# Kernel optimization log

Measured on AMD Instinct MI355X. Metric: run time of the kernel, lower is better.

Reference implementation:

```python
import jax, jax.numpy as jnp
import numpy as np

H, D = 4, 32          # heads, per-head dim (= hidden_channels)
HD = H * D            # concat width fed between layers
L = 2                 # num HGT layers
OUT = 128             # final output dim
SCALE = 1.0 / np.sqrt(D)


def _seg_softmax(score, seg, n):
    # segment softmax over incoming edges per destination node, per head
    mx = jax.ops.segment_max(score, seg, num_segments=n)
    ex = jnp.exp(score - mx[seg])
    den = jax.ops.segment_sum(ex, seg, num_segments=n)
    return ex / den[seg]


def _hgt_side(q_dst, k_src, v_src, src, dst, a_rel, m_rel, p_rel, n_dst):
    # k/v: [N_src,H,D]; a_rel,m_rel: [H,D,D]; p_rel: [H]
    k_t = jnp.einsum('ehd,hdf->ehf', k_src[src], a_rel)          # [E,H,D]
    score = (q_dst[dst] * k_t).sum(-1) * p_rel * SCALE           # [E,H]
    alpha = _seg_softmax(score, dst, n_dst)                      # [E,H]
    v_t = jnp.einsum('ehd,hdf->ehf', v_src[src], m_rel)          # [E,H,D]
    return jax.ops.segment_sum(alpha[..., None] * v_t, dst, num_segments=n_dst)


def _forward(x_m, x_g, W_in_m, b_in_m, W_in_g, b_in_g,
             Wk_m, bk_m, Wq_m, bq_m, Wv_m, bv_m,
             Wk_g, bk_g, Wq_g, bq_g, Wv_g, bv_g,
             a_mg, m_mg, p_mg, a_gm, m_gm, p_gm,
             Wa_m, ba_m, Wa_g, ba_g, skip_m, skip_g,
             W_out_m, b_out_m, W_out_g, b_out_g,
             edge_mg_src, edge_mg_dst, edge_gm_src, edge_gm_dst):
    Nm, Ng = x_m.shape[0], x_g.shape[0]
    # per-node-type input projection
    h_m = x_m @ W_in_m + b_in_m                                  # [Nm,HD]
    h_g = x_g @ W_in_g + b_in_g                                  # [Ng,HD]
    for l in range(L):
        k_m = (h_m @ Wk_m[l] + bk_m[l]).reshape(Nm, H, D)
        q_m = (h_m @ Wq_m[l] + bq_m[l]).reshape(Nm, H, D)
        v_m = (h_m @ Wv_m[l] + bv_m[l]).reshape(Nm, H, D)
        k_g = (h_g @ Wk_g[l] + bk_g[l]).reshape(Ng, H, D)
        q_g = (h_g @ Wq_g[l] + bq_g[l]).reshape(Ng, H, D)
        v_g = (h_g @ Wv_g[l] + bv_g[l]).reshape(Ng, H, D)
        agg_g = _hgt_side(q_g, k_m, v_m, edge_mg_src, edge_mg_dst,
                          a_mg[l], m_mg[l], p_mg[l], Ng)         # [Ng,H,D]
        agg_m = _hgt_side(q_m, k_g, v_g, edge_gm_src, edge_gm_dst,
                          a_gm[l], m_gm[l], p_gm[l], Nm)         # [Nm,H,D]
        o_m = jax.nn.gelu(agg_m.reshape(Nm, HD), approximate=False) @ Wa_m[l] + ba_m[l]
        o_g = jax.nn.gelu(agg_g.reshape(Ng, HD), approximate=False) @ Wa_g[l] + ba_g[l]
        bm = jax.nn.sigmoid(skip_m[l])
        bg = jax.nn.sigmoid(skip_g[l])
        h_m = jax.nn.elu(bm * o_m + (1.0 - bm) * h_m)            # HGTConv skip, then model-level ELU
        h_g = jax.nn.elu(bg * o_g + (1.0 - bg) * h_g)
    out_m = h_m @ W_out_m + b_out_m                              # [Nm,OUT]
    out_g = h_g @ W_out_g + b_out_g                              # [Ng,OUT]
    return jnp.concatenate([out_m, out_g], axis=0)               # [Nm+Ng,OUT]


def setup_inputs() -> dict:
    key = jax.random.key(0)
    ks = iter(jax.random.split(key, 64))
    Nm, Ng, E = 100000, 20000, 500000
    Fm, Fg = 20, 50
    def n(shape, s=0.05):
        return jax.random.normal(next(ks), shape, jnp.float32) * s
    inp = {
        'x_m': n((Nm, Fm), 1.0), 'x_g': n((Ng, Fg), 1.0),
        'W_in_m': n((Fm, HD)), 'b_in_m': jnp.zeros((HD,), jnp.float32),
        'W_in_g': n((Fg, HD)), 'b_in_g': jnp.zeros((HD,), jnp.float32),
        'Wk_m': n((L, HD, HD)), 'bk_m': jnp.zeros((L, HD), jnp.float32),
        'Wq_m': n((L, HD, HD)), 'bq_m': jnp.zeros((L, HD), jnp.float32),
        'Wv_m': n((L, HD, HD)), 'bv_m': jnp.zeros((L, HD), jnp.float32),
        'Wk_g': n((L, HD, HD)), 'bk_g': jnp.zeros((L, HD), jnp.float32),
        'Wq_g': n((L, HD, HD)), 'bq_g': jnp.zeros((L, HD), jnp.float32),
        'Wv_g': n((L, HD, HD)), 'bv_g': jnp.zeros((L, HD), jnp.float32),
        'a_mg': n((L, H, D, D)), 'm_mg': n((L, H, D, D)),
        'p_mg': jnp.ones((L, H), jnp.float32),
        'a_gm': n((L, H, D, D)), 'm_gm': n((L, H, D, D)),
        'p_gm': jnp.ones((L, H), jnp.float32),
        'Wa_m': n((L, HD, HD)), 'ba_m': jnp.zeros((L, HD), jnp.float32),
        'Wa_g': n((L, HD, HD)), 'ba_g': jnp.zeros((L, HD), jnp.float32),
        'skip_m': jnp.ones((L,), jnp.float32), 'skip_g': jnp.ones((L,), jnp.float32),
        'W_out_m': n((HD, OUT)), 'b_out_m': jnp.zeros((OUT,), jnp.float32),
        'W_out_g': n((HD, OUT)), 'b_out_g': jnp.zeros((OUT,), jnp.float32),
        'edge_mg_src': jax.random.randint(next(ks), (E,), 0, Nm, jnp.int32),
        'edge_mg_dst': jax.random.randint(next(ks), (E,), 0, Ng, jnp.int32),
        'edge_gm_src': jax.random.randint(next(ks), (E,), 0, Ng, jnp.int32),
        'edge_gm_dst': jax.random.randint(next(ks), (E,), 0, Nm, jnp.int32),
    }
    return inp


def reference(x_m, x_g, W_in_m, b_in_m, W_in_g, b_in_g,
              Wk_m, bk_m, Wq_m, bq_m, Wv_m, bv_m,
              Wk_g, bk_g, Wq_g, bq_g, Wv_g, bv_g,
              a_mg, m_mg, p_mg, a_gm, m_gm, p_gm,
              Wa_m, ba_m, Wa_g, ba_g, skip_m, skip_g,
              W_out_m, b_out_m, W_out_g, b_out_g,
              edge_mg_src, edge_mg_dst, edge_gm_src, edge_gm_dst):
    return _forward(x_m, x_g, W_in_m, b_in_m, W_in_g, b_in_g,
                    Wk_m, bk_m, Wq_m, bq_m, Wv_m, bv_m,
                    Wk_g, bk_g, Wq_g, bq_g, Wv_g, bv_g,
                    a_mg, m_mg, p_mg, a_gm, m_gm, p_gm,
                    Wa_m, ba_m, Wa_g, ba_g, skip_m, skip_g,
                    W_out_m, b_out_m, W_out_g, b_out_g,
                    edge_mg_src, edge_mg_dst, edge_gm_src, edge_gm_dst)
```

## Files before the change

### kernel.cpp

```cpp
#include <hip/hip_runtime.h>
#include <hip/hip_bf16.h>

#define SCALE_F 0.17677669529663688f

typedef __attribute__((ext_vector_type(8)))  short bfrag;
typedef __attribute__((ext_vector_type(16))) float facc;
typedef __attribute__((ext_vector_type(2)))  float f32x2;

extern "C" __device__ float __ocml_native_exp2_f32(float);

__device__ __forceinline__ float lo16(unsigned u){ return __uint_as_float(u << 16); }
__device__ __forceinline__ float hi16(unsigned u){ return __uint_as_float(u & 0xffff0000u); }
__device__ __forceinline__ float bu2f(unsigned short u){ return __uint_as_float((unsigned)u << 16); }
__device__ __forceinline__ unsigned short f2bu(float f){
    __hip_bfloat16 h = __float2bfloat16(f);
    return *reinterpret_cast<unsigned short*>(&h);
}
__device__ __forceinline__ void storeC(float* p, float v){ *p = v; }
__device__ __forceinline__ void storeC(__hip_bfloat16* p, float v){ *p = __float2bfloat16(v); }

__global__ void hist2_k(const int* __restrict__ d1, int* __restrict__ c1, int E1, int N1,
                        const int* __restrict__ d2, int* __restrict__ c2, int E2, int N2){
    const int* d = blockIdx.y ? d2 : d1;
    int* c = blockIdx.y ? c2 : c1;
    int E = blockIdx.y ? E2 : E1;
    int Nd = blockIdx.y ? N2 : N1;
    int e = blockIdx.x*256 + threadIdx.x;
    if (e >= E) return;
    int dd = d[e];
    if ((unsigned)dd < (unsigned)Nd) atomicAdd(&c[dd], 1);
}

__global__ void scan_block2_k(const int* __restrict__ c1, int* __restrict__ i1, int* __restrict__ b1, int N1,
                              const int* __restrict__ c2, int* __restrict__ i2, int* __restrict__ b2, int N2){
    const int* cnt = blockIdx.y ? c2 : c1;
    int* incl = blockIdx.y ? i2 : i1;
    int* bsum = blockIdx.y ? b2 : b1;
    int N = blockIdx.y ? N2 : N1;
    if ((int)blockIdx.x*256 >= N) return;
    __shared__ int sh[256];
    int tid = threadIdx.x;
    int i = blockIdx.x*256 + tid;
    int v = (i < N) ? cnt[i] : 0;
    sh[tid] = v;
    __syncthreads();
    for (int off = 1; off < 256; off <<= 1){
        int t = (tid >= off) ? sh[tid-off] : 0;
        __syncthreads();
        sh[tid] += t;
        __syncthreads();
    }
    if (i < N) incl[i] = sh[tid];
    if (tid == 255) bsum[blockIdx.x] = sh[255];
}

__global__ void scan_top2_k(int* __restrict__ b1, int nb1, int* __restrict__ b2, int nb2){
    int* bsum = blockIdx.x ? b2 : b1;
    int nb = blockIdx.x ? nb2 : nb1;
    __shared__ int sh[512];
    int tid = threadIdx.x;
    int v = (tid < nb) ? bsum[tid] : 0;
    sh[tid] = v;
    __syncthreads();
    for (int off = 1; off < 512; off <<= 1){
        int t = (tid >= off) ? sh[tid-off] : 0;
        __syncthreads();
        sh[tid] += t;
        __syncthreads();
    }
    if (tid < nb) bsum[tid] = sh[tid] - v;
}

__global__ void finalize2_k(const int* __restrict__ i1, const int* __restrict__ c1,
                            const int* __restrict__ b1, int* __restrict__ p1, int N1, int E1,
                            const int* __restrict__ i2, const int* __restrict__ c2,
                            const int* __restrict__ b2, int* __restrict__ p2, int N2, int E2){
    const int* incl = blockIdx.y ? i2 : i1;
    const int* cnt  = blockIdx.y ? c2 : c1;
    const int* boff = blockIdx.y ? b2 : b1;
    int* indptr = blockIdx.y ? p2 : p1;
    int N = blockIdx.y ? N2 : N1;
    int E = blockIdx.y ? E2 : E1;
    int i = blockIdx.x*256 + threadIdx.x;
    if (i > N) return;
    if (i == N){ indptr[N] = E; return; }
    indptr[i] = boff[i >> 8] + incl[i] - cnt[i];
}

__global__ void scatter2_k(const int* __restrict__ s1, const int* __restrict__ d1,
                           const int* __restrict__ p1, int* __restrict__ u1,
                           int* __restrict__ r1, int E1, int N1,
                           const int* __restrict__ s2, const int* __restrict__ d2,
                           const int* __restrict__ p2, int* __restrict__ u2,
                           int* __restrict__ r2, int E2, int N2){
    const int* src = blockIdx.y ? s2 : s1;
    const int* dst = blockIdx.y ? d2 : d1;
    const int* indptr = blockIdx.y ? p2 : p1;
    int* cur = blockIdx.y ? u2 : u1;
    int* csr = blockIdx.y ? r2 : r1;
    int E = blockIdx.y ? E2 : E1;
    int Nd = blockIdx.y ? N2 : N1;
    int e = blockIdx.x*256 + threadIdx.x;
    if (e >= E) return;
    int d = dst[e];
    if ((unsigned)d >= (unsigned)Nd) return;
    int p = indptr[d] + atomicAdd(&cur[d], 1);
    csr[p] = src[e];
}

template<int K>
__device__ __forceinline__ void in_proj_body(const float* __restrict__ x,
                                             const float* __restrict__ W,
                                             const float* __restrict__ b,
                                             unsigned short* __restrict__ h, int N){
    constexpr int KP4 = (K + 3)/4, KP = KP4*4;
    int j = threadIdx.x;
    float wreg[KP];
    #pragma unroll
    for (int k = 0; k < KP; ++k) wreg[k] = (k < K) ? W[k*128 + j] : 0.f;
    float bj = b[j];
    __shared__ float xs[8][KP];
    for (int base = blockIdx.x*8; base < N; base += gridDim.x*8){
        __syncthreads();
        for (int t = threadIdx.x; t < 8*KP; t += 128){
            int r = t / KP, k = t - r*KP;
            int row = base + r;
            xs[r][k] = (row < N && k < K) ? x[(size_t)row*K + k] : 0.f;
        }
        __syncthreads();
        #pragma unroll
        for (int r = 0; r < 8; ++r){
            int row = base + r;
            if (row >= N) break;
            float acc = bj;
            #pragma unroll
            for (int kk = 0; kk < KP4; ++kk){
                float4 xv = *(const float4*)(&xs[r][kk*4]);
                acc += xv.x*wreg[kk*4] + xv.y*wreg[kk*4+1]
                     + xv.z*wreg[kk*4+2] + xv.w*wreg[kk*4+3];
            }
            h[(size_t)row*128 + j] = f2bu(acc);
        }
    }
}

__global__ __launch_bounds__(128) void in_proj2_k(
    const float* __restrict__ xm, const float* __restrict__ Wm,
    const float* __restrict__ bm_, unsigned short* __restrict__ hm, int Nm,
    const float* __restrict__ xg, const float* __restrict__ Wg,
    const float* __restrict__ bg_, unsigned short* __restrict__ hg, int Ng){
    if (blockIdx.y == 0) in_proj_body<20>(xm, Wm, bm_, hm, Nm);
    else                 in_proj_body<50>(xg, Wg, bg_, hg, Ng);
}

__global__ __launch_bounds__(128) void wprep_k(
    const float* __restrict__ Wq_m, const float* __restrict__ bq_m,
    const float* __restrict__ Wk_m, const float* __restrict__ bk_m,
    const float* __restrict__ Wv_m, const float* __restrict__ bv_m,
    const float* __restrict__ a_mg, const float* __restrict__ m_mg,
    const float* __restrict__ Wq_g, const float* __restrict__ bq_g,
    const float* __restrict__ Wk_g, const float* __restrict__ bk_g,
    const float* __restrict__ Wv_g, const float* __restrict__ bv_g,
    const float* __restrict__ a_gm, const float* __restrict__ m_gm,
    unsigned short* __restrict__ Wtf, float* __restrict__ bfv,
    const float* __restrict__ Wa_m, const float* __restrict__ Wa_g,
    const float* __restrict__ W_out_m, const float* __restrict__ W_out_g,
    unsigned short* __restrict__ Wta, unsigned short* __restrict__ Wtout){
    int b = blockIdx.x;
    if (b < 1536){
        int u = b / 384, j = b % 384;
        int l = u >> 1;  bool sg = (u & 1);
        const float* Wq = (sg ? Wq_g : Wq_m) + l*16384;
        const float* bq = (sg ? bq_g : bq_m) + l*128;
        const float* Wk = (sg ? Wk_g : Wk_m) + l*16384;
        const float* bk = (sg ? bk_g : bk_m) + l*128;
        const float* Wv = (sg ? Wv_g : Wv_m) + l*16384;
        const float* bv = (sg ? bv_g : bv_m) + l*128;
        const float* ar = (sg ? a_gm : a_mg) + l*4096;
        const float* mr = (sg ? m_gm : m_mg) + l*4096;
        unsigned short* Wt = Wtf + (size_t)u*49152;
        float* bf = bfv + u*384;
        int row = threadIdx.x;
        int part = j >> 7, f = j & 127, hh = f >> 5, ff = f & 31;
        float v;
        if (part == 0) v = Wq[row*128 + f];
        else {
            const float* Wx  = (part == 1) ? Wk : Wv;
            const float* rel = (part == 1) ? ar : mr;
            float s = 0.f;
            #pragma unroll
            for (int d = 0; d < 32; ++d)
                s += Wx[row*128 + hh*32 + d] * rel[hh*1024 + d*32 + ff];
            v = s;
        }
        Wt[(size_t)j*128 + row] = f2bu(v);
        if (row == 0){
            float bb;
            if (part == 0) bb = bq[f];
            else {
                const float* bx  = (part == 1) ? bk : bv;
                const float* rel = (part == 1) ? ar : mr;
                float s = 0.f;
                for (int d = 0; d < 32; ++d)
                    s += bx[hh*32 + d] * rel[hh*1024 + d*32 + ff];
                bb = s;
            }
            bf[j] = bb;
        }
    } else {
        int t = b - 1536;
        int y = t >> 7;
        int idx = (t & 127)*128 + threadIdx.x;
        const float* S = (y==0)?Wa_m:(y==1)?Wa_g:(y==2)?(Wa_m+16384):(y==3)?(Wa_g+16384)
                        :(y==4)?W_out_m:W_out_g;
        unsigned short* D = (y==0)?Wta:(y==1)?(Wta+16384):(y==2)?(Wta+32768):(y==3)?(Wta+49152)
                           :(y==4)?Wtout:(Wtout+16384);
        int n = idx >> 7, k = idx & 127;
        D[idx] = f2bu(S[k*128 + n]);
    }
}

template<typename CT, int MODE, int NCHUNK>
__global__ __launch_bounds__(256) void mfma_gemm2(
    const unsigned short* __restrict__ A0, const unsigned short* __restrict__ Wt0,
    const float* __restrict__ bias0, CT* __restrict__ C0, unsigned short* __restrict__ H0,
    int N0, const float* __restrict__ skip0,
    const unsigned short* __restrict__ A1, const unsigned short* __restrict__ Wt1,
    const float* __restrict__ bias1, CT* __restrict__ C1, unsigned short* __restrict__ H1,
    int N1, const float* __restrict__ skip1,
    int ldc, int nblk0){
    bool s0 = ((int)blockIdx.x < nblk0);
    const unsigned short* A  = s0 ? A0 : A1;
    const unsigned short* Wt = s0 ? Wt0 : Wt1;
    const float* bias = s0 ? bias0 : bias1;
    CT* C = s0 ? C0 : C1;
    unsigned short* H = s0 ? H0 : H1;
    int N = s0 ? N0 : N1;
    const float* skip = s0 ? skip0 : skip1;
    int bx = s0 ? blockIdx.x : (blockIdx.x - nblk0);

    __shared__ unsigned short As[64][136];
    __shared__ unsigned short Bs[128][136];
    int tid = threadIdx.x;
    int rb = bx*64;
    #pragma unroll
    for (int ph = 0; ph < 4; ++ph){
        int c = ph*256 + tid;
        int r = c >> 4, off = (c & 15)*8;
        uint4 v = make_uint4(0,0,0,0);
        if (rb + r < N) v = ((const uint4*)(A + (size_t)(rb + r)*128))[c & 15];
        *(uint4*)(&As[r][off]) = v;
    }
    int w = tid >> 6, lane = tid & 63;
    int wr = (w >> 1)*32, wc = (w & 1)*64;
    int m = lane & 31, quad = lane >> 5;
    const unsigned short* ap  = &As[wr + m][quad*8];
    const unsigned short* bp0 = &Bs[wc + m][quad*8];
    const unsigned short* bp1 = &Bs[wc + 32 + m][quad*8];
    float bm = 0.f;
    if (MODE == 2) bm = 1.f/(1.f + __expf(-skip[0]));

    for (int chunk = 0; chunk < NCHUNK; ++chunk){
        int cb = (NCHUNK == 1) ? (int)blockIdx.y*128 : chunk*128;
        if (chunk > 0) __syncthreads();
        #pragma unroll
        for (int ph = 0; ph < 8; ++ph){
            int c = ph*256 + tid;
            int r = c >> 4, off = (c & 15)*8;
            uint4 v = ((const uint4*)(Wt + (size_t)(cb + r)*128))[c & 15];
            *(uint4*)(&Bs[r][off]) = v;
        }
        __syncthreads();
        facc acc0, acc1;
        #pragma unroll
        for (int i = 0; i < 16; ++i){ acc0[i] = 0.f; acc1[i] = 0.f; }
        #pragma unroll
        for (int kc = 0; kc < 8; ++kc){
            bfrag a  = *(const bfrag*)(ap  + kc*16);
            bfrag b0 = *(const bfrag*)(bp0 + kc*16);
            bfrag b1 = *(const bfrag*)(bp1 + kc*16);
            acc0 = __builtin_amdgcn_mfma_f32_32x32x16_bf16(a, b0, acc0, 0, 0, 0);
            acc1 = __builtin_amdgcn_mfma_f32_32x32x16_bf16(a, b1, acc1, 0, 0, 0);
        }
        int col0 = cb + wc + m, col1 = col0 + 32;
        float bias0v = bias[col0], bias1v = bias[col1];
        #pragma unroll
        for (int r = 0; r < 16; ++r){
            int lrow = wr + 4*quad + (r & 3) + 8*(r >> 2);
            int grow = rb + lrow;
            if (grow >= N) continue;
            float o0 = acc0[r] + bias0v;
            float o1 = acc1[r] + bias1v;
            if (MODE == 0){
                storeC(&C[(size_t)grow*ldc + col0], o0);
                storeC(&C[(size_t)grow*ldc + col1], o1);
            } else {
                size_t i0 = (size_t)grow*128 + col0, i1 = (size_t)grow*128 + col1;
                float v0 = bm*o0 + (1.f - bm)*bu2f(H[i0]);
                float v1 = bm*o1 + (1.f - bm)*bu2f(H[i1]);
                v0 = (v0 > 0.f) ? v0 : expm1f(v0);
                v1 = (v1 > 0.f) ? v1 : expm1f(v1);
                H[i0] = f2bu(v0);
                H[i1] = f2bu(v1);
            }
        }
    }
}

__global__ __launch_bounds__(256) void edge_attn5_k(
    const int* __restrict__ ipA, const int* __restrict__ csrA,
    const unsigned short* __restrict__ qdA, const unsigned short* __restrict__ qsA,
    const float* __restrict__ pA, unsigned* __restrict__ aggA, int NdA,
    const int* __restrict__ ipB, const int* __restrict__ csrB,
    const unsigned short* __restrict__ qdB, const unsigned short* __restrict__ qsB,
    const float* __restrict__ pB, unsigned* __restrict__ aggB, int NdB,
    int nblkA){
    bool sA = ((int)blockIdx.x < nblkA);
    const int* ip  = sA ? ipA : ipB;
    const int* csr = sA ? csrA : csrB;
    const unsigned* qd = (const unsigned*)(sA ? qdA : qdB);
    const char* qsc = (const char*)(sA ? qsA : qsB);
    const float* p = sA ? pA : pB;
    unsigned* agg = sA ? aggA : aggB;
    int Nd = sA ? NdA : NdB;
    int bx = sA ? blockIdx.x : (blockIdx.x - nblkA);
    int wid  = (bx << 2) | (threadIdx.x >> 6);
    int lane = threadIdx.x & 63;
    if (wid >= Nd) return;
    int slot = lane >> 4, j = lane & 15;
    float phL = p[j >> 2] * (SCALE_F * 1.4426950408889634f);
    uint4 qv = ((const uint4*)(qd + (size_t)wid*192))[j];
    f32x2 q2[4];
    q2[0] = (f32x2){lo16(qv.x), hi16(qv.x)};
    q2[1] = (f32x2){lo16(qv.y), hi16(qv.y)};
    q2[2] = (f32x2){lo16(qv.z), hi16(qv.z)};
    q2[3] = (f32x2){lo16(qv.w), hi16(qv.w)};
    int beg = ip[wid], end = ip[wid + 1];
    float den = 0.f;
    f32x2 acc2[4] = {};
    int loff = j*16;
    int i0 = beg + slot;
    if (i0 < end){
        int s0c = csr[i0];
        int i1 = i0 + 4;
        bool m1 = (i1 < end);
        int s1 = m1 ? csr[i1] : 0;
        const char* b0 = qsc + (size_t)s0c*768 + loff;
        uint4 kv = *(const uint4*)(b0 + 256);
        uint4 vv = *(const uint4*)(b0 + 512);
        while (true){
            int i2 = i1 + 4;
            bool m2 = (i2 < end);
            int s2 = m2 ? csr[i2] : 0;
            uint4 kv2, vv2;
            if (m1){
                const char* b1 = qsc + (size_t)s1*768 + loff;
                kv2 = *(const uint4*)(b1 + 256);
                vv2 = *(const uint4*)(b1 + 512);
            }
            f32x2 pp = q2[0] * (f32x2){lo16(kv.x), hi16(kv.x)};
            pp += q2[1] * (f32x2){lo16(kv.y), hi16(kv.y)};
            pp += q2[2] * (f32x2){lo16(kv.z), hi16(kv.z)};
            pp += q2[3] * (f32x2){lo16(kv.w), hi16(kv.w)};
            float part = pp.x + pp.y;
            part += __shfl_xor(part, 1);
            part += __shfl_xor(part, 2);
            float e = __ocml_native_exp2_f32(part * phL);
            den += e;
            acc2[0] += (f32x2){lo16(vv.x), hi16(vv.x)} * e;
            acc2[1] += (f32x2){lo16(vv.y), hi16(vv.y)} * e;
            acc2[2] += (f32x2){lo16(vv.z), hi16(vv.z)} * e;
            acc2[3] += (f32x2){lo16(vv.w), hi16(vv.w)} * e;
            if (!m1) break;
            kv = kv2; vv = vv2;
            i1 = i2; m1 = m2; s1 = s2;
        }
    }
    den += __shfl_xor(den, 16);
    den += __shfl_xor(den, 32);
    #pragma unroll
    for (int k = 0; k < 4; ++k){
        f32x2 t;
        t.x = __shfl_xor(acc2[k].x, 16);
        t.y = __shfl_xor(acc2[k].y, 16);
        acc2[k] += t;
        t.x = __shfl_xor(acc2[k].x, 32);
        t.y = __shfl_xor(acc2[k].y, 32);
        acc2[k] += t;
    }
    float inv = (den > 0.f) ? 1.f/den : 0.f;
    f32x2 sel = (slot & 2) ? ((slot & 1) ? acc2[3] : acc2[2])
                           : ((slot & 1) ? acc2[1] : acc2[0]);
    float o0 = sel.x*inv, o1 = sel.y*inv;
    o0 = 0.5f*o0*(1.f + erff(o0*0.70710678118654752f));
    o1 = 0.5f*o1*(1.f + erff(o1*0.70710678118654752f));
    agg[(size_t)wid*64 + j*4 + slot] = (unsigned)f2bu(o0) | ((unsigned)f2bu(o1) << 16);
}

extern "C" void kernel_launch(void* const* d_in, const int* in_sizes, int n_in,
                              void* d_out, int out_size, void* d_ws, size_t ws_size,
                              hipStream_t stream){
    typedef const float* FP;
    FP x_m = (FP)d_in[0], x_g = (FP)d_in[1];
    FP W_in_m = (FP)d_in[2], b_in_m = (FP)d_in[3], W_in_g = (FP)d_in[4], b_in_g = (FP)d_in[5];
    FP Wk_m = (FP)d_in[6],  bk_m = (FP)d_in[7],  Wq_m = (FP)d_in[8],  bq_m = (FP)d_in[9];
    FP Wv_m = (FP)d_in[10], bv_m = (FP)d_in[11];
    FP Wk_g = (FP)d_in[12], bk_g = (FP)d_in[13], Wq_g = (FP)d_in[14], bq_g = (FP)d_in[15];
    FP Wv_g = (FP)d_in[16], bv_g = (FP)d_in[17];
    FP a_mg = (FP)d_in[18], m_mg = (FP)d_in[19], p_mg = (FP)d_in[20];
    FP a_gm = (FP)d_in[21], m_gm = (FP)d_in[22], p_gm = (FP)d_in[23];
    FP Wa_m = (FP)d_in[24], ba_m = (FP)d_in[25], Wa_g = (FP)d_in[26], ba_g = (FP)d_in[27];
    FP skip_m = (FP)d_in[28], skip_g = (FP)d_in[29];
    FP W_out_m = (FP)d_in[30], b_out_m = (FP)d_in[31], W_out_g = (FP)d_in[32], b_out_g = (FP)d_in[33];
    const int* e_mg_src = (const int*)d_in[34];
    const int* e_mg_dst = (const int*)d_in[35];
    const int* e_gm_src = (const int*)d_in[36];
    const int* e_gm_dst = (const int*)d_in[37];

    const int Nm = in_sizes[0] / 20;
    const int Ng = in_sizes[1] / 50;
    const int E1 = in_sizes[34];
    const int E2 = in_sizes[36];

    char* wp = (char*)d_ws;
    auto alloc = [&](size_t bytes) -> char* {
        char* r = wp; wp += (bytes + 255) & ~(size_t)255; return r;
    };
    unsigned short* h_m   = (unsigned short*)alloc((size_t)Nm*128*2);
    unsigned short* h_g   = (unsigned short*)alloc((size_t)Ng*128*2);
    unsigned short* agg_m = (unsigned short*)alloc((size_t)Nm*128*2);
    unsigned short* agg_g = (unsigned short*)alloc((size_t)Ng*128*2);
    unsigned short* qkv_m = (unsigned short*)alloc((size_t)Nm*384*2);
    unsigned short* qkv_g = (unsigned short*)alloc((size_t)Ng*384*2);
    unsigned short* Wtf   = (unsigned short*)alloc((size_t)4*49152*2);
    float*          bfv   = (float*)alloc((size_t)4*384*4);
    unsigned short* Wta   = (unsigned short*)alloc((size_t)4*16384*2);
    unsigned short* Wtout = (unsigned short*)alloc((size_t)2*16384*2);
    int* indptr_g = (int*)alloc((size_t)(Ng+1)*4);
    int* csr_mg   = (int*)alloc((size_t)E1*4);
    int* indptr_m = (int*)alloc((size_t)(Nm+1)*4);
    int* csr_gm   = (int*)alloc((size_t)E2*4);
    int maxN = Nm > Ng ? Nm : Ng;
    int* cnt  = (int*)alloc((size_t)maxN*4);
    int* cur  = (int*)alloc((size_t)maxN*4);
    int* cnt2 = (int*)alloc((size_t)maxN*4);
    int* cur2 = (int*)alloc((size_t)maxN*4);
    int* incl = (int*)alloc((size_t)maxN*4);
    int* incl2= (int*)alloc((size_t)maxN*4);
    int* bsum = (int*)alloc(512*4);
    int* bsum2= (int*)alloc(512*4);

    size_t used = (size_t)(wp - (char*)d_ws);
    if (used > ws_size){
        hipMemsetAsync(d_out, 0, (size_t)out_size*4, stream);
        return;
    }
    hipMemsetAsync(cnt, 0, (size_t)((char*)cur2 - (char*)cnt) + (size_t)maxN*4, stream);

    int maxE = E1 > E2 ? E1 : E2;
    int nb1 = (Ng + 255)/256, nb2 = (Nm + 255)/256;
    int nbmax = nb1 > nb2 ? nb1 : nb2;
    hist2_k<<<dim3((maxE + 255)/256, 2), 256, 0, stream>>>(
        e_mg_dst, cnt, E1, Ng, e_gm_dst, cnt2, E2, Nm);
    scan_block2_k<<<dim3(nbmax, 2), 256, 0, stream>>>(
        cnt, incl, bsum, Ng, cnt2, incl2, bsum2, Nm);
    scan_top2_k<<<2, 512, 0, stream>>>(bsum, nb1, bsum2, nb2);
    finalize2_k<<<dim3(nbmax + 1, 2), 256, 0, stream>>>(
        incl, cnt, bsum, indptr_g, Ng, E1, incl2, cnt2, bsum2, indptr_m, Nm, E2);
    scatter2_k<<<dim3((maxE + 255)/256, 2), 256, 0, stream>>>(
        e_mg_src, e_mg_dst, indptr_g, cur, csr_mg, E1, Ng,
        e_gm_src, e_gm_dst, indptr_m, cur2, csr_gm, E2, Nm);

    wprep_k<<<2304, 128, 0, stream>>>(
        Wq_m, bq_m, Wk_m, bk_m, Wv_m, bv_m, a_mg, m_mg,
        Wq_g, bq_g, Wk_g, bk_g, Wv_g, bv_g, a_gm, m_gm,
        Wtf, bfv, Wa_m, Wa_g, W_out_m, W_out_g, Wta, Wtout);

    in_proj2_k<<<dim3(2048, 2), 128, 0, stream>>>(
        x_m, W_in_m, b_in_m, h_m, Nm,
        x_g, W_in_g, b_in_g, h_g, Ng);

    int gxm = (Nm + 63)/64, gxg = (Ng + 63)/64;
    int nbA = (Ng + 3)/4, nbB = (Nm + 3)/4;

    for (int l = 0; l < 2; ++l){
        mfma_gemm2<__hip_bfloat16, 0, 3><<<dim3(gxm + gxg, 1), 256, 0, stream>>>(
            h_m, Wtf + (size_t)(l*2+0)*49152, bfv + (l*2+0)*384,
            (__hip_bfloat16*)qkv_m, nullptr, Nm, nullptr,
            h_g, Wtf + (size_t)(l*2+1)*49152, bfv + (l*2+1)*384,
            (__hip_bfloat16*)qkv_g, nullptr, Ng, nullptr,
            384, gxm);

        edge_attn5_k<<<nbA + nbB, 256, 0, stream>>>(
            indptr_g, csr_mg, qkv_g, qkv_m, p_mg + l*4, (unsigned*)agg_g, Ng,
            indptr_m, csr_gm, qkv_m, qkv_g, p_gm + l*4, (unsigned*)agg_m, Nm,
            nbA);

        mfma_gemm2<float, 2, 1><<<dim3(gxm + gxg, 1), 256, 0, stream>>>(
            agg_m, Wta + (size_t)(l*2+0)*16384, ba_m + l*128, (float*)nullptr, h_m, Nm, skip_m + l,
            agg_g, Wta + (size_t)(l*2+1)*16384, ba_g + l*128, (float*)nullptr, h_g, Ng, skip_g + l,
            128, gxm);
    }

    float* outp = (float*)d_out;
    mfma_gemm2<float, 0, 1><<<dim3(gxm + gxg, 1), 256, 0, stream>>>(
        h_m, Wtout, b_out_m, outp, nullptr, Nm, nullptr,
        h_g, Wtout + 16384, b_out_g, outp + (size_t)Nm*128, nullptr, Ng, nullptr,
        128, gxm);
}
```

Before: 595.0 us.

## Split QKV into separate Q and packed KV buffers, narrow GEMM column tile

The QKV projection GEMM now writes Q to its own [N,128] buffer and K/V to a packed [N,256] buffer through a new epilogue mode. The edge attention kernel then gathers K and V from a 512-byte row stride instead of 768 bytes. The intent is to make per-edge source gathers denser and cache-friendlier. The GEMM tile also narrows from 128 to 64 output columns per chunk, with one accumulator per wave and a smaller B tile in LDS. That lowers register and LDS use, but each block now loops over more chunks and reloads B more often.

```diff
diff --git a/kernel.cpp b/kernel.cpp
--- a/kernel.cpp
+++ b/kernel.cpp
@@ -16,8 +16,6 @@
     __hip_bfloat16 h = __float2bfloat16(f);
     return *reinterpret_cast<unsigned short*>(&h);
 }
-__device__ __forceinline__ void storeC(float* p, float v){ *p = v; }
-__device__ __forceinline__ void storeC(__hip_bfloat16* p, float v){ *p = __float2bfloat16(v); }
 
 __global__ void hist2_k(const int* __restrict__ d1, int* __restrict__ c1, int E1, int N1,
                         const int* __restrict__ d2, int* __restrict__ c2, int E2, int N2){
@@ -240,7 +238,7 @@
     int bx = s0 ? blockIdx.x : (blockIdx.x - nblk0);
 
     __shared__ unsigned short As[64][136];
-    __shared__ unsigned short Bs[128][136];
+    __shared__ unsigned short Bs[64][136];
     int tid = threadIdx.x;
     int rb = bx*64;
     #pragma unroll
@@ -252,74 +250,70 @@
         *(uint4*)(&As[r][off]) = v;
     }
     int w = tid >> 6, lane = tid & 63;
-    int wr = (w >> 1)*32, wc = (w & 1)*64;
+    int wr = (w >> 1)*32, wc = (w & 1)*32;
     int m = lane & 31, quad = lane >> 5;
-    const unsigned short* ap  = &As[wr + m][quad*8];
-    const unsigned short* bp0 = &Bs[wc + m][quad*8];
-    const unsigned short* bp1 = &Bs[wc + 32 + m][quad*8];
+    const unsigned short* ap = &As[wr + m][quad*8];
+    const unsigned short* bp = &Bs[wc + m][quad*8];
     float bm = 0.f;
     if (MODE == 2) bm = 1.f/(1.f + __expf(-skip[0]));
 
     for (int chunk = 0; chunk < NCHUNK; ++chunk){
-        int cb = (NCHUNK == 1) ? (int)blockIdx.y*128 : chunk*128;
+        int cb = chunk*64;
         if (chunk > 0) __syncthreads();
         #pragma unroll
-        for (int ph = 0; ph < 8; ++ph){
+        for (int ph = 0; ph < 4; ++ph){
             int c = ph*256 + tid;
             int r = c >> 4, off = (c & 15)*8;
             uint4 v = ((const uint4*)(Wt + (size_t)(cb + r)*128))[c & 15];
             *(uint4*)(&Bs[r][off]) = v;
         }
         __syncthreads();
-        facc acc0, acc1;
+        facc acc;
         #pragma unroll
-        for (int i = 0; i < 16; ++i){ acc0[i] = 0.f; acc1[i] = 0.f; }
+        for (int i = 0; i < 16; ++i) acc[i] = 0.f;
         #pragma unroll
         for (int kc = 0; kc < 8; ++kc){
-            bfrag a  = *(const bfrag*)(ap  + kc*16);
-            bfrag b0 = *(const bfrag*)(bp0 + kc*16);
-            bfrag b1 = *(const bfrag*)(bp1 + kc*16);
-            acc0 = __builtin_amdgcn_mfma_f32_32x32x16_bf16(a, b0, acc0, 0, 0, 0);
-            acc1 = __builtin_amdgcn_mfma_f32_32x32x16_bf16(a, b1, acc1, 0, 0, 0);
-        }
-        int col0 = cb + wc + m, col1 = col0 + 32;
-        float bias0v = bias[col0], bias1v = bias[col1];
+            bfrag a = *(const bfrag*)(ap + kc*16);
+            bfrag b = *(const bfrag*)(bp + kc*16);
+            acc = __builtin_amdgcn_mfma_f32_32x32x16_bf16(a, b, acc, 0, 0, 0);
+        }
+        int col = cb + wc + m;
+        float biasv = bias[col];
         #pragma unroll
         for (int r = 0; r < 16; ++r){
             int lrow = wr + 4*quad + (r & 3) + 8*(r >> 2);
             int grow = rb + lrow;
             if (grow >= N) continue;
-            float o0 = acc0[r] + bias0v;
-            float o1 = acc1[r] + bias1v;
+            float o = acc[r] + biasv;
             if (MODE == 0){
-                storeC(&C[(size_t)grow*ldc + col0], o0);
-                storeC(&C[(size_t)grow*ldc + col1], o1);
+                C[(size_t)grow*ldc + col] = (CT)o;
+            } else if (MODE == 1){
+                unsigned short* qp  = (unsigned short*)C;
+                if (col < 128) qp[(size_t)grow*128 + col] = f2bu(o);
+                else           H[(size_t)grow*256 + (col - 128)] = f2bu(o);
             } else {
-                size_t i0 = (size_t)grow*128 + col0, i1 = (size_t)grow*128 + col1;
-                float v0 = bm*o0 + (1.f - bm)*bu2f(H[i0]);
-                float v1 = bm*o1 + (1.f - bm)*bu2f(H[i1]);
+                size_t i0 = (size_t)grow*128 + col;
+                float v0 = bm*o + (1.f - bm)*bu2f(H[i0]);
                 v0 = (v0 > 0.f) ? v0 : expm1f(v0);
-                v1 = (v1 > 0.f) ? v1 : expm1f(v1);
                 H[i0] = f2bu(v0);
-                H[i1] = f2bu(v1);
             }
         }
     }
 }
 
-__global__ __launch_bounds__(256) void edge_attn5_k(
+__global__ __launch_bounds__(256) void edge_attn7_k(
     const int* __restrict__ ipA, const int* __restrict__ csrA,
-    const unsigned short* __restrict__ qdA, const unsigned short* __restrict__ qsA,
+    const unsigned short* __restrict__ qdA, const unsigned short* __restrict__ kvA,
     const float* __restrict__ pA, unsigned* __restrict__ aggA, int NdA,
     const int* __restrict__ ipB, const int* __restrict__ csrB,
-    const unsigned short* __restrict__ qdB, const unsigned short* __restrict__ qsB,
+    const unsigned short* __restrict__ qdB, const unsigned short* __restrict__ kvB,
     const float* __restrict__ pB, unsigned* __restrict__ aggB, int NdB,
     int nblkA){
     bool sA = ((int)blockIdx.x < nblkA);
     const int* ip  = sA ? ipA : ipB;
     const int* csr = sA ? csrA : csrB;
-    const unsigned* qd = (const unsigned*)(sA ? qdA : qdB);
-    const char* qsc = (const char*)(sA ? qsA : qsB);
+    const uint4* qd = (const uint4*)(sA ? qdA : qdB);
+    const char* kvc = (const char*)(sA ? kvA : kvB);
     const float* p = sA ? pA : pB;
     unsigned* agg = sA ? aggA : aggB;
     int Nd = sA ? NdA : NdB;
@@ -329,7 +323,7 @@
     if (wid >= Nd) return;
     int slot = lane >> 4, j = lane & 15;
     float phL = p[j >> 2] * (SCALE_F * 1.4426950408889634f);
-    uint4 qv = ((const uint4*)(qd + (size_t)wid*192))[j];
+    uint4 qv = qd[(size_t)wid*16 + j];
     f32x2 q2[4];
     q2[0] = (f32x2){lo16(qv.x), hi16(qv.x)};
     q2[1] = (f32x2){lo16(qv.y), hi16(qv.y)};
@@ -345,18 +339,18 @@
         int i1 = i0 + 4;
         bool m1 = (i1 < end);
         int s1 = m1 ? csr[i1] : 0;
-        const char* b0 = qsc + (size_t)s0c*768 + loff;
-        uint4 kv = *(const uint4*)(b0 + 256);
-        uint4 vv = *(const uint4*)(b0 + 512);
+        const char* b0 = kvc + (size_t)s0c*512 + loff;
+        uint4 kv = *(const uint4*)(b0);
+        uint4 vv = *(const uint4*)(b0 + 256);
         while (true){
             int i2 = i1 + 4;
             bool m2 = (i2 < end);
             int s2 = m2 ? csr[i2] : 0;
             uint4 kv2, vv2;
             if (m1){
-                const char* b1 = qsc + (size_t)s1*768 + loff;
-                kv2 = *(const uint4*)(b1 + 256);
-                vv2 = *(const uint4*)(b1 + 512);
+                const char* b1 = kvc + (size_t)s1*512 + loff;
+                kv2 = *(const uint4*)(b1);
+                vv2 = *(const uint4*)(b1 + 256);
             }
             f32x2 pp = q2[0] * (f32x2){lo16(kv.x), hi16(kv.x)};
             pp += q2[1] * (f32x2){lo16(kv.y), hi16(kv.y)};
@@ -430,8 +424,10 @@
     unsigned short* h_g   = (unsigned short*)alloc((size_t)Ng*128*2);
     unsigned short* agg_m = (unsigned short*)alloc((size_t)Nm*128*2);
     unsigned short* agg_g = (unsigned short*)alloc((size_t)Ng*128*2);
-    unsigned short* qkv_m = (unsigned short*)alloc((size_t)Nm*384*2);
-    unsigned short* qkv_g = (unsigned short*)alloc((size_t)Ng*384*2);
+    unsigned short* q_m   = (unsigned short*)alloc((size_t)Nm*128*2);
+    unsigned short* kv_m  = (unsigned short*)alloc((size_t)Nm*256*2);
+    unsigned short* q_g   = (unsigned short*)alloc((size_t)Ng*128*2);
+    unsigned short* kv_g  = (unsigned short*)alloc((size_t)Ng*256*2);
     unsigned short* Wtf   = (unsigned short*)alloc((size_t)4*49152*2);
     float*          bfv   = (float*)alloc((size_t)4*384*4);
     unsigned short* Wta   = (unsigned short*)alloc((size_t)4*16384*2);
@@ -484,26 +480,26 @@
     int nbA = (Ng + 3)/4, nbB = (Nm + 3)/4;
 
     for (int l = 0; l < 2; ++l){
-        mfma_gemm2<__hip_bfloat16, 0, 3><<<dim3(gxm + gxg, 1), 256, 0, stream>>>(
+        mfma_gemm2<__hip_bfloat16, 1, 6><<<dim3(gxm + gxg, 1), 256, 0, stream>>>(
             h_m, Wtf + (size_t)(l*2+0)*49152, bfv + (l*2+0)*384,
-            (__hip_bfloat16*)qkv_m, nullptr, Nm, nullptr,
+            (__hip_bfloat16*)q_m, kv_m, Nm, nullptr,
             h_g, Wtf + (size_t)(l*2+1)*49152, bfv + (l*2+1)*384,
-            (__hip_bfloat16*)qkv_g, nullptr, Ng, nullptr,
-            384, gxm);
-
-        edge_attn5_k<<<nbA + nbB, 256, 0, stream>>>(
-            indptr_g, csr_mg, qkv_g, qkv_m, p_mg + l*4, (unsigned*)agg_g, Ng,
-            indptr_m, csr_gm, qkv_m, qkv_g, p_gm + l*4, (unsigned*)agg_m, Nm,
+            (__hip_bfloat16*)q_g, kv_g, Ng, nullptr,
+            0, gxm);
+
+        edge_attn7_k<<<nbA + nbB, 256, 0, stream>>>(
+            indptr_g, csr_mg, q_g, kv_m, p_mg + l*4, (unsigned*)agg_g, Ng,
+            indptr_m, csr_gm, q_m, kv_g, p_gm + l*4, (unsigned*)agg_m, Nm,
             nbA);
 
-        mfma_gemm2<float, 2, 1><<<dim3(gxm + gxg, 1), 256, 0, stream>>>(
+        mfma_gemm2<float, 2, 2><<<dim3(gxm + gxg, 1), 256, 0, stream>>>(
             agg_m, Wta + (size_t)(l*2+0)*16384, ba_m + l*128, (float*)nullptr, h_m, Nm, skip_m + l,
             agg_g, Wta + (size_t)(l*2+1)*16384, ba_g + l*128, (float*)nullptr, h_g, Ng, skip_g + l,
             128, gxm);
     }
 
     float* outp = (float*)d_out;
-    mfma_gemm2<float, 0, 1><<<dim3(gxm + gxg, 1), 256, 0, stream>>>(
+    mfma_gemm2<float, 0, 2><<<dim3(gxm + gxg, 1), 256, 0, stream>>>(
         h_m, Wtout, b_out_m, outp, nullptr, Nm, nullptr,
         h_g, Wtout + 16384, b_out_g, outp + (size_t)Nm*128, nullptr, Ng, nullptr,
         128, gxm);
```

Result: no change. 604.3 us (+1.6%).

## Split QKV output into separate Q and packed KV buffers; prefetch weight chunks

Applied to the files above, without the earlier changes.

The QKV projection GEMM gets a new store mode that writes Q to its own [N,128] buffer and K/V to a packed [N,256] buffer. The edge attention kernel then gathers K and V from 512-byte rows instead of strided 768-byte rows, so the random per-edge source reads skip the unused Q segment and have a smaller footprint. The GEMM also preloads the next 128-column weight chunk into registers while the current chunk is computed, overlapping global loads with MFMA work. This costs more registers in the GEMM and a branch in the epilogue store.

```diff
diff --git a/kernel.cpp b/kernel.cpp
--- a/kernel.cpp
+++ b/kernel.cpp
@@ -260,15 +260,22 @@
     float bm = 0.f;
     if (MODE == 2) bm = 1.f/(1.f + __expf(-skip[0]));
 
+    int brow = tid >> 4, bidx = tid & 15, boff = bidx*8;
+    uint4 breg[8];
+    #pragma unroll
+    for (int ph = 0; ph < 8; ++ph)
+        breg[ph] = ((const uint4*)(Wt + (size_t)(ph*16 + brow)*128))[bidx];
+
+    #pragma unroll
     for (int chunk = 0; chunk < NCHUNK; ++chunk){
-        int cb = (NCHUNK == 1) ? (int)blockIdx.y*128 : chunk*128;
         if (chunk > 0) __syncthreads();
         #pragma unroll
-        for (int ph = 0; ph < 8; ++ph){
-            int c = ph*256 + tid;
-            int r = c >> 4, off = (c & 15)*8;
-            uint4 v = ((const uint4*)(Wt + (size_t)(cb + r)*128))[c & 15];
-            *(uint4*)(&Bs[r][off]) = v;
+        for (int ph = 0; ph < 8; ++ph)
+            *(uint4*)(&Bs[ph*16 + brow][boff]) = breg[ph];
+        if (chunk + 1 < NCHUNK){
+            #pragma unroll
+            for (int ph = 0; ph < 8; ++ph)
+                breg[ph] = ((const uint4*)(Wt + (size_t)((chunk+1)*128 + ph*16 + brow)*128))[bidx];
         }
         __syncthreads();
         facc acc0, acc1;
@@ -282,6 +289,7 @@
             acc0 = __builtin_amdgcn_mfma_f32_32x32x16_bf16(a, b0, acc0, 0, 0, 0);
             acc1 = __builtin_amdgcn_mfma_f32_32x32x16_bf16(a, b1, acc1, 0, 0, 0);
         }
+        int cb = chunk*128;
         int col0 = cb + wc + m, col1 = col0 + 32;
         float bias0v = bias[col0], bias1v = bias[col1];
         #pragma unroll
@@ -294,6 +302,15 @@
             if (MODE == 0){
                 storeC(&C[(size_t)grow*ldc + col0], o0);
                 storeC(&C[(size_t)grow*ldc + col1], o1);
+            } else if (MODE == 1){
+                unsigned short* qp = (unsigned short*)C;
+                if (col0 < 128){
+                    qp[(size_t)grow*128 + col0] = f2bu(o0);
+                    qp[(size_t)grow*128 + col1] = f2bu(o1);
+                } else {
+                    H[(size_t)grow*256 + (col0 - 128)] = f2bu(o0);
+                    H[(size_t)grow*256 + (col1 - 128)] = f2bu(o1);
+                }
             } else {
                 size_t i0 = (size_t)grow*128 + col0, i1 = (size_t)grow*128 + col1;
                 float v0 = bm*o0 + (1.f - bm)*bu2f(H[i0]);
@@ -307,19 +324,19 @@
     }
 }
 
-__global__ __launch_bounds__(256) void edge_attn5_k(
+__global__ __launch_bounds__(256) void edge_attn7_k(
     const int* __restrict__ ipA, const int* __restrict__ csrA,
-    const unsigned short* __restrict__ qdA, const unsigned short* __restrict__ qsA,
+    const unsigned short* __restrict__ qdA, const unsigned short* __restrict__ kvA,
     const float* __restrict__ pA, unsigned* __restrict__ aggA, int NdA,
     const int* __restrict__ ipB, const int* __restrict__ csrB,
-    const unsigned short* __restrict__ qdB, const unsigned short* __restrict__ qsB,
+    const unsigned short* __restrict__ qdB, const unsigned short* __restrict__ kvB,
     const float* __restrict__ pB, unsigned* __restrict__ aggB, int NdB,
     int nblkA){
     bool sA = ((int)blockIdx.x < nblkA);
     const int* ip  = sA ? ipA : ipB;
     const int* csr = sA ? csrA : csrB;
-    const unsigned* qd = (const unsigned*)(sA ? qdA : qdB);
-    const char* qsc = (const char*)(sA ? qsA : qsB);
+    const uint4* qd = (const uint4*)(sA ? qdA : qdB);
+    const char* kvc = (const char*)(sA ? kvA : kvB);
     const float* p = sA ? pA : pB;
     unsigned* agg = sA ? aggA : aggB;
     int Nd = sA ? NdA : NdB;
@@ -329,7 +346,7 @@
     if (wid >= Nd) return;
     int slot = lane >> 4, j = lane & 15;
     float phL = p[j >> 2] * (SCALE_F * 1.4426950408889634f);
-    uint4 qv = ((const uint4*)(qd + (size_t)wid*192))[j];
+    uint4 qv = qd[(size_t)wid*16 + j];
     f32x2 q2[4];
     q2[0] = (f32x2){lo16(qv.x), hi16(qv.x)};
     q2[1] = (f32x2){lo16(qv.y), hi16(qv.y)};
@@ -345,18 +362,18 @@
         int i1 = i0 + 4;
         bool m1 = (i1 < end);
         int s1 = m1 ? csr[i1] : 0;
-        const char* b0 = qsc + (size_t)s0c*768 + loff;
-        uint4 kv = *(const uint4*)(b0 + 256);
-        uint4 vv = *(const uint4*)(b0 + 512);
+        const char* b0 = kvc + (size_t)s0c*512 + loff;
+        uint4 kv = *(const uint4*)(b0);
+        uint4 vv = *(const uint4*)(b0 + 256);
         while (true){
             int i2 = i1 + 4;
             bool m2 = (i2 < end);
             int s2 = m2 ? csr[i2] : 0;
             uint4 kv2, vv2;
             if (m1){
-                const char* b1 = qsc + (size_t)s1*768 + loff;
-                kv2 = *(const uint4*)(b1 + 256);
-                vv2 = *(const uint4*)(b1 + 512);
+                const char* b1 = kvc + (size_t)s1*512 + loff;
+                kv2 = *(const uint4*)(b1);
+                vv2 = *(const uint4*)(b1 + 256);
             }
             f32x2 pp = q2[0] * (f32x2){lo16(kv.x), hi16(kv.x)};
             pp += q2[1] * (f32x2){lo16(kv.y), hi16(kv.y)};
@@ -430,8 +447,10 @@
     unsigned short* h_g   = (unsigned short*)alloc((size_t)Ng*128*2);
     unsigned short* agg_m = (unsigned short*)alloc((size_t)Nm*128*2);
     unsigned short* agg_g = (unsigned short*)alloc((size_t)Ng*128*2);
-    unsigned short* qkv_m = (unsigned short*)alloc((size_t)Nm*384*2);
-    unsigned short* qkv_g = (unsigned short*)alloc((size_t)Ng*384*2);
+    unsigned short* q_m   = (unsigned short*)alloc((size_t)Nm*128*2);
+    unsigned short* kv_m  = (unsigned short*)alloc((size_t)Nm*256*2);
+    unsigned short* q_g   = (unsigned short*)alloc((size_t)Ng*128*2);
+    unsigned short* kv_g  = (unsigned short*)alloc((size_t)Ng*256*2);
     unsigned short* Wtf   = (unsigned short*)alloc((size_t)4*49152*2);
     float*          bfv   = (float*)alloc((size_t)4*384*4);
     unsigned short* Wta   = (unsigned short*)alloc((size_t)4*16384*2);
@@ -484,16 +503,16 @@
     int nbA = (Ng + 3)/4, nbB = (Nm + 3)/4;
 
     for (int l = 0; l < 2; ++l){
-        mfma_gemm2<__hip_bfloat16, 0, 3><<<dim3(gxm + gxg, 1), 256, 0, stream>>>(
+        mfma_gemm2<__hip_bfloat16, 1, 3><<<dim3(gxm + gxg, 1), 256, 0, stream>>>(
             h_m, Wtf + (size_t)(l*2+0)*49152, bfv + (l*2+0)*384,
-            (__hip_bfloat16*)qkv_m, nullptr, Nm, nullptr,
+            (__hip_bfloat16*)q_m, kv_m, Nm, nullptr,
             h_g, Wtf + (size_t)(l*2+1)*49152, bfv + (l*2+1)*384,
-            (__hip_bfloat16*)qkv_g, nullptr, Ng, nullptr,
-            384, gxm);
-
-        edge_attn5_k<<<nbA + nbB, 256, 0, stream>>>(
-            indptr_g, csr_mg, qkv_g, qkv_m, p_mg + l*4, (unsigned*)agg_g, Ng,
-            indptr_m, csr_gm, qkv_m, qkv_g, p_gm + l*4, (unsigned*)agg_m, Nm,
+            (__hip_bfloat16*)q_g, kv_g, Ng, nullptr,
+            0, gxm);
+
+        edge_attn7_k<<<nbA + nbB, 256, 0, stream>>>(
+            indptr_g, csr_mg, q_g, kv_m, p_mg + l*4, (unsigned*)agg_g, Ng,
+            indptr_m, csr_gm, q_m, kv_g, p_gm + l*4, (unsigned*)agg_m, Nm,
             nbA);
 
         mfma_gemm2<float, 2, 1><<<dim3(gxm + gxg, 1), 256, 0, stream>>>(
```

After: 651.0 us. +9.4%, slower.
